# Performance work log

Measured on AMD Instinct MI355X. Metric: run time of the kernel, lower is better.

## Reference

```python
import jax, jax.numpy as jnp
import numpy as np

B, CIN, COUT, RES_IN, RES, LDIM = 16, 512, 512, 32, 64, 512
SQ2 = float(np.sqrt(2.0))   # relu def_gain
SQH = float(np.sqrt(0.5))   # residual gain
DN = ('NCHW', 'OIHW', 'NCHW')


def _f2d():
    # setup_filter([1,3,3,1]): normalize to sum 1, separable -> outer product
    f = jnp.array([1.0, 3.0, 3.0, 1.0], jnp.float32)
    f = f / f.sum()
    return jnp.outer(f, f)  # [4,4]


def _upfirdn(x, f2d, up, pad):
    # upfirdn2d: zero-upsample by `up` (zeros appended after each sample),
    # pad (pad0,pad1) per side, correlate with depthwise 4-tap filter.
    # lhs_dilation yields (H-1)*up+1, so fold the trailing up-1 zeros into right pad.
    C = x.shape[1]
    k = jnp.broadcast_to(f2d[None, None], (C, 1, 4, 4))
    p = (pad[0], pad[1] + up - 1)
    return jax.lax.conv_general_dilated(
        x, k, (1, 1), [p, p], lhs_dilation=(up, up),
        dimension_numbers=DN, feature_group_count=C)


def _affine(lat, w, b):
    # FullyConnectedLayer: weight_gain = 1/sqrt(in_features), bias_init handled in setup
    return lat @ (w * (1.0 / np.sqrt(w.shape[1]))).T + b


def _mod_demod(x, w, style):
    # modulate input, compute demod coefs: rsqrt(sum_i,k,k (w[o,i]*s[b,i])^2 + 1e-8)
    xm = x * style[:, :, None, None]
    d = jax.lax.rsqrt(
        jnp.einsum('bi,oi->bo', style * style, jnp.sum(w * w, axis=(2, 3))) + 1e-8)
    return xm, d


def setup_inputs():
    key = jax.random.key(0)
    ks = jax.random.split(key, 12)
    n = lambda k, s: jax.random.normal(k, s, jnp.float32)
    return dict(
        x=n(ks[0], (B, CIN, RES_IN, RES_IN)),
        latent1=n(ks[1], (B, 1, LDIM)),
        latent2=n(ks[2], (B, 2, LDIM)),
        aff0_w=n(ks[3], (CIN, LDIM)), aff0_b=jnp.ones((CIN,), jnp.float32),
        w0=n(ks[4], (COUT, CIN, 3, 3)), b0=jnp.zeros((COUT,), jnp.float32),
        nc0=n(ks[5], (RES, RES)), ns0=0.1 * n(ks[6], ()),
        aff1_w=n(ks[7], (COUT, LDIM)), aff1_b=jnp.ones((COUT,), jnp.float32),
        w1=n(ks[8], (COUT, COUT, 3, 3)), b1=jnp.zeros((COUT,), jnp.float32),
        nc1=n(ks[9], (RES, RES)), ns1=0.1 * n(ks[10], ()),
        skip_w=n(ks[11], (COUT, CIN, 1, 1)),
    )


def reference(x, latent1, latent2, aff0_w, aff0_b, w0, b0, nc0, ns0,
              aff1_w, aff1_b, w1, b1, nc1, ns1, skip_w):
    f2d = _f2d()
    # --- skip branch: Conv2dLayer(k=1, up=2, bias=False), gain sqrt(0.5) ---
    # conv2d_resample fast path: upfirdn(up=2, pad=(2,1), gain=up^2) then 1x1 conv
    xs = _upfirdn(x, f2d * 4.0, up=2, pad=(2, 1))              # [B,CIN,64,64]
    ws = skip_w * (1.0 / np.sqrt(CIN))                          # weight_gain, k=1
    y = jax.lax.conv_general_dilated(xs, ws, (1, 1), [(0, 0), (0, 0)],
                                     dimension_numbers=DN) * SQH
    # --- conv0: SynthesisLayer up=2 (modulated transposed conv + FIR) ---
    s0 = _affine(latent2[:, 0], aff0_w, aff0_b)                 # [B,CIN]
    h, d0 = _mod_demod(x, w0, s0)
    # torch conv_transpose2d(x, w0.T(0,1), stride=2, pad=0) == dilated conv,
    # pad k-1=2, kernel spatially flipped (flip_weight=False path)
    h = jax.lax.conv_general_dilated(h, jnp.flip(w0, (2, 3)), (1, 1),
                                     [(2, 2), (2, 2)], lhs_dilation=(2, 2),
                                     dimension_numbers=DN)      # [B,COUT,65,65]
    h = _upfirdn(h, f2d * 4.0, up=1, pad=(1, 1))                # [B,COUT,64,64]
    h = h * d0[:, :, None, None] + nc0 * ns0                    # demod + noise (fma)
    h = jax.nn.relu(h + b0[None, :, None, None]) * SQ2          # bias_act
    # --- conv1: SynthesisLayer up=1, gain sqrt(0.5) ---
    s1 = _affine(latent2[:, 1], aff1_w, aff1_b)                 # [B,COUT]
    h, d1 = _mod_demod(h, w1, s1)
    h = jax.lax.conv_general_dilated(h, w1, (1, 1), [(1, 1), (1, 1)],
                                     dimension_numbers=DN)
    h = h * d1[:, :, None, None] + nc1 * ns1
    h = jax.nn.relu(h + b1[None, :, None, None]) * (SQ2 * SQH)
    return y + h
```

## Files before the change

### kernel.cpp

```cpp
#include <hip/hip_runtime.h>
#include <hip/hip_bf16.h>


typedef __attribute__((ext_vector_type(8))) short short8;
typedef __attribute__((ext_vector_type(4))) float floatx4;

__device__ __forceinline__ float bf2f(__hip_bfloat16 v){ return __bfloat162float(v); }
__device__ __forceinline__ __hip_bfloat16 f2bf(float v){ return __float2bfloat16(v); }

__device__ __forceinline__ void glds16(const __hip_bfloat16* g, const short* l){
  __builtin_amdgcn_global_load_lds(
      (const __attribute__((address_space(1))) void*)g,
      (__attribute__((address_space(3))) void*)l,
      16, 0, 0);
}

__device__ __forceinline__ float ldin(const void* p, size_t i, int f32){
  return f32 ? ((const float*)p)[i] : bf2f(((const __hip_bfloat16*)p)[i]);
}

__global__ void k_detect(const void* __restrict__ x, int* __restrict__ flag){
  __shared__ int cnt;
  if (threadIdx.x == 0) cnt = 0;
  __syncthreads();
  const __hip_bfloat16* xb = (const __hip_bfloat16*)x;
  int c = 0;
  for (int i = threadIdx.x; i < 4096; i += 256){
    float v = bf2f(xb[i]);
    if (!(fabsf(v) < 1e6f)) c++;
  }
  atomicAdd(&cnt, c);
  __syncthreads();
  if (threadIdx.x == 0) *flag = (cnt > 8) ? 1 : 0;
}

__global__ void k_misc(const void* __restrict__ nc0, const void* __restrict__ nc1,
                       const void* __restrict__ b0,  const void* __restrict__ b1,
                       const void* __restrict__ ns0, const void* __restrict__ ns1,
                       const int* __restrict__ flag,
                       float* __restrict__ nf0, float* __restrict__ nf1,
                       float* __restrict__ b0f, float* __restrict__ b1f,
                       float* __restrict__ scf, float* __restrict__ zbuf){
  const int f32 = *flag;
  int i = blockIdx.x*256 + threadIdx.x;
  if (i < 4096)       nf0[i]      = ldin(nc0, i, f32);
  else if (i < 8192)  nf1[i-4096] = ldin(nc1, i-4096, f32);
  else if (i < 8704)  b0f[i-8192] = ldin(b0, i-8192, f32);
  else if (i < 9216)  b1f[i-8704] = ldin(b1, i-8704, f32);
  else if (i == 9216) scf[0]      = ldin(ns0, 0, f32);
  else if (i == 9217) scf[1]      = ldin(ns1, 0, f32);
  else if (i >= 9232 && i < 9744) zbuf[i-9232] = 0.0f;
}


__global__ void k_wsum(const void* __restrict__ w0, const void* __restrict__ w1,
                       const int* __restrict__ flag,
                       float* __restrict__ wsum0, float* __restrict__ wsum1){
  const int f32 = *flag;
  int idx = blockIdx.x*256 + threadIdx.x;
  float a = 0.f, b = 0.f;
  #pragma unroll
  for(int t=0;t<9;t++){
    float v0 = ldin(w0, (size_t)idx*9+t, f32); a += v0*v0;
    float v1 = ldin(w1, (size_t)idx*9+t, f32); b += v1*v1;
  }
  wsum0[idx] = a; wsum1[idx] = b;
}

__global__ void k_styles(const void* __restrict__ lat2,
                         const void* __restrict__ aw0, const void* __restrict__ ab0,
                         const void* __restrict__ aw1, const void* __restrict__ ab1,
                         const int* __restrict__ flag,
                         float* __restrict__ s0, float* __restrict__ s1){
  const int f32 = *flag;
  int idx = blockIdx.x*256 + threadIdx.x;
  if (idx >= 16*512) return;
  int b = idx>>9, o = idx&511;
  float a0 = 0.f, a1 = 0.f;
  for(int i=0;i<512;i++){
    a0 += ldin(lat2, (size_t)b*1024 + i,       f32) * ldin(aw0, (size_t)o*512+i, f32);
    a1 += ldin(lat2, (size_t)b*1024 + 512 + i, f32) * ldin(aw1, (size_t)o*512+i, f32);
  }
  const float inv = 0.04419417382415922f;
  s0[idx] = a0*inv + ldin(ab0, o, f32);
  s1[idx] = a1*inv + ldin(ab1, o, f32);
}

__global__ void k_demod(const float* __restrict__ s0, const float* __restrict__ s1,
                        const float* __restrict__ wsum0, const float* __restrict__ wsum1,
                        float* __restrict__ d0, float* __restrict__ d1){
  int idx = blockIdx.x*256 + threadIdx.x;
  if (idx >= 16*512) return;
  int b = idx>>9, o = idx&511;
  float a0 = 0.f, a1 = 0.f;
  for(int i=0;i<512;i++){
    float t0 = s0[b*512+i]; a0 += t0*t0*wsum0[o*512+i];
    float t1 = s1[b*512+i]; a1 += t1*t1*wsum1[o*512+i];
  }
  d0[idx] = rsqrtf(a0 + 1e-8f);
  d1[idx] = rsqrtf(a1 + 1e-8f);
}

__global__ void k_xprep(const void* __restrict__ x, const int* __restrict__ flag,
                        __hip_bfloat16* __restrict__ xT){
  const int f32 = *flag;
  int tid = blockIdx.x*256 + threadIdx.x;
  int ci = tid&511; int r = tid>>9;
  int xx = r&31; r >>= 5; int yy = r&31; int b = r>>5;
  xT[tid] = f2bf(ldin(x, (size_t)(((b*512+ci)*32+yy)*32+xx), f32));
}

__global__ void k_xmod(__hip_bfloat16* __restrict__ xT,
                       const float* __restrict__ s0){
  int tid = blockIdx.x*256 + threadIdx.x;
  int ci = tid&511; int b = tid>>19;
  xT[tid] = f2bf(bf2f(xT[tid]) * s0[b*512+ci]);
}

__global__ void k_w0prep(const void* __restrict__ w0, const int* __restrict__ flag,
                         __hip_bfloat16* __restrict__ W0p){
  const int f32 = *flag;
  int idx = blockIdx.x*256 + threadIdx.x;
  int oc = idx>>9, ci = idx&511;
  const float g[4] = {0.25f, 0.75f, 0.75f, 0.25f};
  float K2[6][6] = {};
  #pragma unroll
  for(int ty=0;ty<3;ty++)
    #pragma unroll
    for(int tx=0;tx<3;tx++){
      float w = ldin(w0, (size_t)idx*9 + (2-ty)*3 + (2-tx), f32);
      #pragma unroll
      for(int qy=0;qy<4;qy++)
        #pragma unroll
        for(int qx=0;qx<4;qx++)
          K2[qy+ty][qx+tx] += g[qy]*g[qx]*w;
    }
  #pragma unroll
  for(int Py=0;Py<2;Py++)
    #pragma unroll
    for(int Px=0;Px<2;Px++){
      int cls = Py*2+Px;
      #pragma unroll
      for(int jy=0;jy<3;jy++)
        #pragma unroll
        for(int jx=0;jx<3;jx++){
          int sy = (1-Py) + 2*jy, sx = (1-Px) + 2*jx;
          W0p[((size_t)(cls*9 + jy*3+jx)*512 + oc)*512 + ci] = f2bf(K2[sy][sx]);
        }
    }
}

__global__ void k_w1prep(const void* __restrict__ w1, const void* __restrict__ skw,
                         const int* __restrict__ flag,
                         __hip_bfloat16* __restrict__ w1T,
                         __hip_bfloat16* __restrict__ wskipT){
  const int f32 = *flag;
  int idx = blockIdx.x*256 + threadIdx.x;
  int oc = idx>>9, ci = idx&511;
  #pragma unroll
  for(int t=0;t<9;t++)
    w1T[((size_t)t*512 + oc)*512 + ci] = f2bf(ldin(w1, (size_t)idx*9+t, f32));
  wskipT[idx] = f2bf(ldin(skw, idx, f32) * 0.03125f);
}

template<int TAPS, int MODE, int H>
__launch_bounds__(256,4)
__global__ void k_gemm(const __hip_bfloat16* __restrict__ Ain,
                       const __hip_bfloat16* __restrict__ Wt,
                       const float* __restrict__ dvec,
                       const float* __restrict__ noise,
                       const float* __restrict__ nscal,
                       const float* __restrict__ bias,
                       const float* __restrict__ s1,
                       const __hip_bfloat16* __restrict__ tlow,
                       const __hip_bfloat16* __restrict__ zbuf,
                       void* __restrict__ Outv){
  constexpr int LOGH = (H==32)?5:6;
  __shared__ short As[128*32];
  __shared__ short Bs[128*32];
  const int t = threadIdx.x;
  const int mtile = ((blockIdx.x & 7) * (gridDim.x >> 3)) + (blockIdx.x >> 3);
  const int Mbase = mtile*128;
  const int Nbase = blockIdx.y*128;
  const int cls = blockIdx.z;
  const __hip_bfloat16* Wslab = Wt + (size_t)cls * TAPS * 512 * 512;

  const int wave = t>>6, lane = t&63;
  const int wm = (wave>>1)*64, wn = (wave&1)*64;
  const int lm = lane&15, lk = (lane>>4)*8;

  const int rsub = lane>>2;
  const int koff = (lane&3)*8;
  const int row0 = wave*16 + rsub;
  const int row1 = row0 + 64;
  short* ldsA0 = As + wave*512;
  short* ldsA1 = As + (wave+4)*512;
  short* ldsB0 = Bs + wave*512;
  short* ldsB1 = Bs + (wave+4)*512;

  floatx4 acc[4][4];
  #pragma unroll
  for(int i=0;i<4;i++)
    #pragma unroll
    for(int j=0;j<4;j++)
      #pragma unroll
      for(int r=0;r<4;r++) acc[i][j][r] = 0.0f;

  const int m0 = Mbase + row0, m1 = Mbase + row1;
  const int b0p = m0 >> (2*LOGH), b1p = m1 >> (2*LOGH);
  const int py0 = (m0 >> LOGH)&(H-1), py1 = (m1 >> LOGH)&(H-1);
  const int px0 = m0 & (H-1),        px1 = m1 & (H-1);

  #pragma unroll 1
  for(int tap=0; tap<TAPS; ++tap){
    const int dy = (TAPS==1)?0:(tap/3 - 1);
    const int dx = (TAPS==1)?0:(tap%3 - 1);
    const int iy0 = py0+dy, ix0 = px0+dx, iy1 = py1+dy, ix1 = px1+dx;
    const bool v0 = ((unsigned)iy0 < (unsigned)H) && ((unsigned)ix0 < (unsigned)H);
    const bool v1 = ((unsigned)iy1 < (unsigned)H) && ((unsigned)ix1 < (unsigned)H);
    const __hip_bfloat16* pA0 = v0 ? (Ain + ((((b0p*H + iy0)*H + ix0) << 9) + koff))
                                   : (zbuf + koff);
    const __hip_bfloat16* pA1 = v1 ? (Ain + ((((b1p*H + iy1)*H + ix1) << 9) + koff))
                                   : (zbuf + koff);
    const __hip_bfloat16* wt  = Wslab + (size_t)tap*512*512;
    const __hip_bfloat16* pB0 = wt + (Nbase + row0)*512 + koff;
    const __hip_bfloat16* pB1 = wt + (Nbase + row1)*512 + koff;

    #pragma unroll 1
    for(int kk=0; kk<512; kk+=32){
      glds16(pA0, ldsA0);
      glds16(pA1, ldsA1);
      glds16(pB0, ldsB0);
      glds16(pB1, ldsB1);
      __syncthreads();
      short8 af[4], bf[4];
      #pragma unroll
      for(int i=0;i<4;i++) af[i] = *(const short8*)&As[(wm + i*16 + lm)*32 + lk];
      #pragma unroll
      for(int j=0;j<4;j++) bf[j] = *(const short8*)&Bs[(wn + j*16 + lm)*32 + lk];
      #pragma unroll
      for(int i=0;i<4;i++)
        #pragma unroll
        for(int j=0;j<4;j++)
          acc[i][j] = __builtin_amdgcn_mfma_f32_16x16x32_bf16(af[i], bf[j], acc[i][j], 0,0,0);
      __syncthreads();
      pA0 += 32; pA1 += 32; pB0 += 32; pB1 += 32;
    }
  }

  const float nsv = (MODE>=1) ? nscal[0] : 0.0f;
  #pragma unroll
  for(int i=0;i<4;i++){
    #pragma unroll
    for(int j=0;j<4;j++){
      const int mt = Mbase + wm + i*16 + (lane>>4)*4;
      const int n  = Nbase + wn + j*16 + lm;
      #pragma unroll
      for(int r=0;r<4;r++){
        const int m = mt + r;
        float val = acc[i][j][r];
        if constexpr (MODE==0){
          ((__hip_bfloat16*)Outv)[(size_t)m*512 + n] = f2bf(val);
        } else if constexpr (MODE==1){
          const int b = m>>10, uy = (m>>5)&31, ux = m&31;
          const int py = 2*uy + (cls>>1), px = 2*ux + (cls&1);
          val = val*dvec[b*512+n] + noise[py*64+px]*nsv + bias[n];
          val = fmaxf(val, 0.0f) * 1.4142135623730951f * s1[b*512+n];
          ((__hip_bfloat16*)Outv)[(size_t)((b*64+py)*64+px)*512 + n] = f2bf(val);
        } else {
          const int b = m>>12, py = (m>>6)&63, px = m&63;
          val = val*dvec[b*512+n] + noise[py*64+px]*nsv + bias[n];
          val = fmaxf(val, 0.0f);
          const int uy = py>>1, ay = py&1, ux2 = px>>1, ax = px&1;
          const int ry = uy - 1 + ay, rx = ux2 - 1 + ax;
          const float cy0 = ay ? 0.75f : 0.25f, cy1 = ay ? 0.25f : 0.75f;
          const float cx0 = ax ? 0.75f : 0.25f, cx1 = ax ? 0.25f : 0.75f;
          float yv = 0.0f;
          #pragma unroll
          for(int e=0;e<2;e++){
            const int yy = ry + e;
            if ((unsigned)yy >= 32u) continue;
            const float cy = e ? cy1 : cy0;
            #pragma unroll
            for(int f=0;f<2;f++){
              const int xx = rx + f;
              if ((unsigned)xx >= 32u) continue;
              const float cx = f ? cx1 : cx0;
              yv += cy*cx*bf2f(tlow[(size_t)((b*32+yy)*32+xx)*512 + n]);
            }
          }
          val += yv;
          ((float*)Outv)[(size_t)((b*512 + n)*64 + py)*64 + px] = val;
        }
      }
    }
  }
}


extern "C" void kernel_launch(void* const* d_in, const int* in_sizes, int n_in,
                              void* d_out, int out_size, void* d_ws, size_t ws_size,
                              hipStream_t stream){
  (void)in_sizes; (void)n_in; (void)out_size; (void)ws_size;
  const void* x    = d_in[0];
  const void* lat2 = d_in[2];
  const void* aw0  = d_in[3];
  const void* ab0  = d_in[4];
  const void* w0   = d_in[5];
  const void* b0   = d_in[6];
  const void* nc0  = d_in[7];
  const void* ns0  = d_in[8];
  const void* aw1  = d_in[9];
  const void* ab1  = d_in[10];
  const void* w1   = d_in[11];
  const void* b1   = d_in[12];
  const void* nc1  = d_in[13];
  const void* ns1  = d_in[14];
  const void* skw  = d_in[15];

  char* p = (char*)d_ws;
  float* s0v   = (float*)p; p += 16*512*4;
  float* s1v   = (float*)p; p += 16*512*4;
  float* d0v   = (float*)p; p += 16*512*4;
  float* d1v   = (float*)p; p += 16*512*4;
  float* nf0   = (float*)p; p += 4096*4;
  float* nf1   = (float*)p; p += 4096*4;
  float* b0f   = (float*)p; p += 512*4;
  float* b1f   = (float*)p; p += 512*4;
  float* scf   = (float*)p; p += 16;
  int*   flag  = (int*)p;   p += 16;
  float* zbuf  = (float*)p; p += 512*4;
  __hip_bfloat16* w1T    = (__hip_bfloat16*)p; p += (size_t)9*512*512*2;
  __hip_bfloat16* wskipT = (__hip_bfloat16*)p; p += (size_t)512*512*2;
  __hip_bfloat16* tlow   = (__hip_bfloat16*)p; p += (size_t)16*32*32*512*2;
  __hip_bfloat16* xT     = (__hip_bfloat16*)p; p += (size_t)16*32*32*512*2;
  __hip_bfloat16* W0p    = (__hip_bfloat16*)p; p += (size_t)4*9*512*512*2;
  __hip_bfloat16* act0m  = (__hip_bfloat16*)p; p += (size_t)16*64*64*512*2;
  float* wsum0 = (float*)act0m;
  float* wsum1 = (float*)act0m + 512*512;

  const __hip_bfloat16* zb = (const __hip_bfloat16*)zbuf;

  k_detect<<<   1, 256, 0, stream>>>(x, flag);
  k_misc  <<<  39, 256, 0, stream>>>(nc0, nc1, b0, b1, ns0, ns1, flag,
                                     nf0, nf1, b0f, b1f, scf, zbuf);
  k_wsum  <<<1024, 256, 0, stream>>>(w0, w1, flag, wsum0, wsum1);
  k_styles<<<  32, 256, 0, stream>>>(lat2, aw0, ab0, aw1, ab1, flag, s0v, s1v);
  k_demod <<<  32, 256, 0, stream>>>(s0v, s1v, wsum0, wsum1, d0v, d1v);
  k_xprep <<<32768,256, 0, stream>>>(x, flag, xT);
  k_w0prep<<<1024, 256, 0, stream>>>(w0, flag, W0p);
  k_w1prep<<<1024, 256, 0, stream>>>(w1, skw, flag, w1T, wskipT);

  k_gemm<1,0,32><<<dim3(128,4,1), 256, 0, stream>>>(
      xT, wskipT, nullptr, nullptr, nullptr, nullptr, nullptr, nullptr, zb, tlow);
  k_xmod  <<<32768,256, 0, stream>>>(xT, s0v);
  k_gemm<9,1,32><<<dim3(128,4,4), 256, 0, stream>>>(
      xT, W0p, d0v, nf0, scf, b0f, s1v, nullptr, zb, act0m);
  k_gemm<9,2,64><<<dim3(512,4,1), 256, 0, stream>>>(
      act0m, w1T, d1v, nf1, scf+1, b1f, nullptr, tlow, zb, d_out);
}
```

Measured before the change: 1.560 ms.

## Load GEMM operands directly from global memory into MFMA registers, dropping LDS staging

The implicit-GEMM kernel stops staging A and B tiles in shared memory with global_load_lds and barriers. Each lane now loads its MFMA fragments straight from global memory, and the K loop is fully unrolled. This removes LDS traffic and both __syncthreads per K step. In exchange, waves that share rows or columns no longer share loaded data, so each tile element is fetched several times through L1/L2, and register pressure rises from the full unroll.

```diff
diff --git a/kernel.cpp b/kernel.cpp
--- a/kernel.cpp
+++ b/kernel.cpp
@@ -7,13 +7,6 @@
 
 __device__ __forceinline__ float bf2f(__hip_bfloat16 v){ return __bfloat162float(v); }
 __device__ __forceinline__ __hip_bfloat16 f2bf(float v){ return __float2bfloat16(v); }
-
-__device__ __forceinline__ void glds16(const __hip_bfloat16* g, const short* l){
-  __builtin_amdgcn_global_load_lds(
-      (const __attribute__((address_space(1))) void*)g,
-      (__attribute__((address_space(3))) void*)l,
-      16, 0, 0);
-}
 
 __device__ __forceinline__ float ldin(const void* p, size_t i, int f32){
   return f32 ? ((const float*)p)[i] : bf2f(((const __hip_bfloat16*)p)[i]);
@@ -176,8 +169,6 @@
                        const __hip_bfloat16* __restrict__ zbuf,
                        void* __restrict__ Outv){
   constexpr int LOGH = (H==32)?5:6;
-  __shared__ short As[128*32];
-  __shared__ short Bs[128*32];
   const int t = threadIdx.x;
   const int mtile = ((blockIdx.x & 7) * (gridDim.x >> 3)) + (blockIdx.x >> 3);
   const int Mbase = mtile*128;
@@ -187,16 +178,8 @@
 
   const int wave = t>>6, lane = t&63;
   const int wm = (wave>>1)*64, wn = (wave&1)*64;
-  const int lm = lane&15, lk = (lane>>4)*8;
-
-  const int rsub = lane>>2;
-  const int koff = (lane&3)*8;
-  const int row0 = wave*16 + rsub;
-  const int row1 = row0 + 64;
-  short* ldsA0 = As + wave*512;
-  short* ldsA1 = As + (wave+4)*512;
-  short* ldsB0 = Bs + wave*512;
-  short* ldsB1 = Bs + (wave+4)*512;
+  const int lm = lane&15;
+  const int lkq = (lane>>4)*8;
 
   floatx4 acc[4][4];
   #pragma unroll
@@ -206,45 +189,47 @@
       #pragma unroll
       for(int r=0;r<4;r++) acc[i][j][r] = 0.0f;
 
-  const int m0 = Mbase + row0, m1 = Mbase + row1;
-  const int b0p = m0 >> (2*LOGH), b1p = m1 >> (2*LOGH);
-  const int py0 = (m0 >> LOGH)&(H-1), py1 = (m1 >> LOGH)&(H-1);
-  const int px0 = m0 & (H-1),        px1 = m1 & (H-1);
+  int bI[4], pyI[4], pxI[4];
+  #pragma unroll
+  for(int i=0;i<4;i++){
+    const int m = Mbase + wm + i*16 + lm;
+    bI[i]  = m >> (2*LOGH);
+    pyI[i] = (m >> LOGH) & (H-1);
+    pxI[i] = m & (H-1);
+  }
+  const __hip_bfloat16* pB[4];
+  #pragma unroll
+  for(int j=0;j<4;j++)
+    pB[j] = Wslab + (((Nbase + wn + j*16 + lm) << 9) + lkq);
 
   #pragma unroll 1
   for(int tap=0; tap<TAPS; ++tap){
     const int dy = (TAPS==1)?0:(tap/3 - 1);
     const int dx = (TAPS==1)?0:(tap%3 - 1);
-    const int iy0 = py0+dy, ix0 = px0+dx, iy1 = py1+dy, ix1 = px1+dx;
-    const bool v0 = ((unsigned)iy0 < (unsigned)H) && ((unsigned)ix0 < (unsigned)H);
-    const bool v1 = ((unsigned)iy1 < (unsigned)H) && ((unsigned)ix1 < (unsigned)H);
-    const __hip_bfloat16* pA0 = v0 ? (Ain + ((((b0p*H + iy0)*H + ix0) << 9) + koff))
-                                   : (zbuf + koff);
-    const __hip_bfloat16* pA1 = v1 ? (Ain + ((((b1p*H + iy1)*H + ix1) << 9) + koff))
-                                   : (zbuf + koff);
-    const __hip_bfloat16* wt  = Wslab + (size_t)tap*512*512;
-    const __hip_bfloat16* pB0 = wt + (Nbase + row0)*512 + koff;
-    const __hip_bfloat16* pB1 = wt + (Nbase + row1)*512 + koff;
-
-    #pragma unroll 1
+    const __hip_bfloat16* pA[4];
+    #pragma unroll
+    for(int i=0;i<4;i++){
+      const int iy = pyI[i] + dy, ix = pxI[i] + dx;
+      const bool v = ((unsigned)iy < (unsigned)H) && ((unsigned)ix < (unsigned)H);
+      pA[i] = v ? (Ain + ((((size_t)(bI[i]*H + iy)*H + ix) << 9) + lkq))
+                : (zbuf + lkq);
+    }
+    const __hip_bfloat16* wtap = (TAPS==1) ? nullptr : (const __hip_bfloat16*)0;
+    (void)wtap;
+    const size_t tof = (size_t)tap * 262144;
+
+    #pragma unroll
     for(int kk=0; kk<512; kk+=32){
-      glds16(pA0, ldsA0);
-      glds16(pA1, ldsA1);
-      glds16(pB0, ldsB0);
-      glds16(pB1, ldsB1);
-      __syncthreads();
-      short8 af[4], bf[4];
-      #pragma unroll
-      for(int i=0;i<4;i++) af[i] = *(const short8*)&As[(wm + i*16 + lm)*32 + lk];
-      #pragma unroll
-      for(int j=0;j<4;j++) bf[j] = *(const short8*)&Bs[(wn + j*16 + lm)*32 + lk];
+      short8 a[4], bb[4];
+      #pragma unroll
+      for(int i=0;i<4;i++) a[i]  = *(const short8*)(pA[i] + kk);
+      #pragma unroll
+      for(int j=0;j<4;j++) bb[j] = *(const short8*)(pB[j] + tof + kk);
       #pragma unroll
       for(int i=0;i<4;i++)
         #pragma unroll
         for(int j=0;j<4;j++)
-          acc[i][j] = __builtin_amdgcn_mfma_f32_16x16x32_bf16(af[i], bf[j], acc[i][j], 0,0,0);
-      __syncthreads();
-      pA0 += 32; pA1 += 32; pB0 += 32; pB1 += 32;
+          acc[i][j] = __builtin_amdgcn_mfma_f32_16x16x32_bf16(a[i], bb[j], acc[i][j], 0,0,0);
     }
   }
 
```

Measured after the change: 2.719 ms. +74.4%, slower.
